# Optimization experiments

Measured on AMD Instinct MI355X. Metric: run time of the kernel, lower is better.

The kernel has to match this reference:

```python
import jax, jax.numpy as jnp
import numpy as np

D_MODEL = 1024
N_HEADS = 16
HEAD_DIM = D_MODEL // N_HEADS
D_FF = 4096
LN_EPS = 1e-5


def _layernorm(x, g, b):
    mu = jnp.mean(x, axis=-1, keepdims=True)
    var = jnp.var(x, axis=-1, keepdims=True)
    return (x - mu) * jax.lax.rsqrt(var + LN_EPS) * g + b


def setup_inputs() -> dict:
    key = jax.random.key(0)
    ks = jax.random.split(key, 10)
    s = 0.02
    return {
        "hidden_states": jax.random.normal(ks[0], (2, 2048, D_MODEL), dtype=jnp.float32),
        "qkv_w": jax.random.normal(ks[1], (3 * D_MODEL, D_MODEL), dtype=jnp.float32) * s,
        "qkv_b": jnp.zeros((3 * D_MODEL,), dtype=jnp.float32),
        "out_w": jax.random.normal(ks[2], (D_MODEL, D_MODEL), dtype=jnp.float32) * s,
        "out_b": jnp.zeros((D_MODEL,), dtype=jnp.float32),
        "fc1_w": jax.random.normal(ks[3], (D_FF, D_MODEL), dtype=jnp.float32) * s,
        "fc1_b": jnp.zeros((D_FF,), dtype=jnp.float32),
        "fc2_w": jax.random.normal(ks[4], (D_MODEL, D_FF), dtype=jnp.float32) * s,
        "fc2_b": jnp.zeros((D_MODEL,), dtype=jnp.float32),
        "ln1_g": jnp.ones((D_MODEL,), dtype=jnp.float32),
        "ln1_b": jnp.zeros((D_MODEL,), dtype=jnp.float32),
        "ln2_g": jnp.ones((D_MODEL,), dtype=jnp.float32),
        "ln2_b": jnp.zeros((D_MODEL,), dtype=jnp.float32),
    }


def reference(hidden_states, qkv_w, qkv_b, out_w, out_b, fc1_w, fc1_b, fc2_w, fc2_b, ln1_g, ln1_b, ln2_g, ln2_b):
    B, S, D = hidden_states.shape
    scale = 1.0 / np.sqrt(HEAD_DIM).astype(np.float32)

    normed = _layernorm(hidden_states, ln1_g, ln1_b)
    qkv = normed @ qkv_w.T + qkv_b  # [B,S,3D]
    qkv = qkv.reshape(B, S, 3, N_HEADS, HEAD_DIM).transpose(2, 0, 3, 1, 4)
    q, k, v = qkv[0], qkv[1], qkv[2]  # [B,H,S,hd]

    scores = jnp.einsum("bhqd,bhkd->bhqk", q, k) * scale
    causal = jnp.tril(jnp.ones((S, S), dtype=bool))
    scores = jnp.where(causal, scores, jnp.float32(-jnp.inf))
    probs = jax.nn.softmax(scores, axis=-1)
    attn = jnp.einsum("bhqk,bhkd->bhqd", probs, v)  # [B,H,S,hd]
    attn = attn.transpose(0, 2, 1, 3).reshape(B, S, D)
    attn = attn @ out_w.T + out_b

    hidden = hidden_states + attn
    normed2 = _layernorm(hidden, ln2_g, ln2_b)
    ff = jax.nn.gelu(normed2 @ fc1_w.T + fc1_b, approximate=False)
    ff = ff @ fc2_w.T + fc2_b
    return hidden + ff
```

## Files before the change

### kernel.cpp

```cpp
#include <hip/hip_runtime.h>
#include <math.h>

using bf16   = __bf16;
using bf16x8 = __attribute__((ext_vector_type(8))) __bf16;
using bf16x4 = __attribute__((ext_vector_type(4))) __bf16;
using f32x4  = __attribute__((ext_vector_type(4))) float;
using f32x16 = __attribute__((ext_vector_type(16))) float;

#define MFMA_16x16x32(a, b, c) __builtin_amdgcn_mfma_f32_16x16x32_bf16((a), (b), (c), 0, 0, 0)
#define MFMA32(a, b, c) __builtin_amdgcn_mfma_f32_32x32x16_bf16((a), (b), (c), 0, 0, 0)

__device__ __forceinline__ void gll16(const void* g, void* l) {
  __builtin_amdgcn_global_load_lds((const __attribute__((address_space(1))) void*)g,
                                   (__attribute__((address_space(3))) void*)l,
                                   16, 0, 0);
}

__device__ __forceinline__ int cvtpk(float lo, float hi) {
  int r;
  asm("v_cvt_pk_bf16_f32 %0, %1, %2" : "=v"(r) : "v"(lo), "v"(hi));
  return r;
}

__global__ __launch_bounds__(256) void cast4_kernel(const float* __restrict__ s0, bf16* d0,
                                                    const float* __restrict__ s1, bf16* d1,
                                                    const float* __restrict__ s2, bf16* d2,
                                                    const float* __restrict__ s3, bf16* d3) {
  int i = blockIdx.x * 256 + threadIdx.x;
  const float* s;
  bf16* d;
  if (i < 786432) { s = s0; d = d0; }
  else if (i < 1048576) { s = s1; d = d1; i -= 786432; }
  else if (i < 2097152) { s = s2; d = d2; i -= 1048576; }
  else { s = s3; d = d3; i -= 2097152; }
  float4 v = ((const float4*)s)[i];
  bf16x4 o;
  o[0] = (bf16)v.x; o[1] = (bf16)v.y; o[2] = (bf16)v.z; o[3] = (bf16)v.w;
  ((bf16x4*)d)[i] = o;
}

__global__ __launch_bounds__(256) void ln_kernel(const float* __restrict__ x,
                                                 const float* __restrict__ g,
                                                 const float* __restrict__ b,
                                                 bf16* __restrict__ out) {
  const int row = blockIdx.x, t = threadIdx.x;
  const float4 v = ((const float4*)(x + (size_t)row * 1024))[t];
  float s1 = v.x + v.y + v.z + v.w;
  float s2 = v.x * v.x + v.y * v.y + v.z * v.z + v.w * v.w;
#pragma unroll
  for (int d = 32; d; d >>= 1) {
    s1 += __shfl_xor(s1, d);
    s2 += __shfl_xor(s2, d);
  }
  __shared__ float red[8];
  const int w = t >> 6;
  if ((t & 63) == 0) { red[w] = s1; red[4 + w] = s2; }
  __syncthreads();
  s1 = red[0] + red[1] + red[2] + red[3];
  s2 = red[4] + red[5] + red[6] + red[7];
  const float mu = s1 * (1.f / 1024.f);
  const float rstd = rsqrtf(s2 * (1.f / 1024.f) - mu * mu + 1e-5f);
  const float4 gv = ((const float4*)g)[t];
  const float4 bv = ((const float4*)b)[t];
  bf16x4 o;
  o[0] = (bf16)((v.x - mu) * rstd * gv.x + bv.x);
  o[1] = (bf16)((v.y - mu) * rstd * gv.y + bv.y);
  o[2] = (bf16)((v.z - mu) * rstd * gv.z + bv.z);
  o[3] = (bf16)((v.w - mu) * rstd * gv.w + bv.w);
  ((bf16x4*)(out + (size_t)row * 1024))[t] = o;
}

template <int EPI>
__global__ __launch_bounds__(512, 2) void gemm256(const bf16* __restrict__ A,
                                                  const bf16* __restrict__ W,
                                                  const float* __restrict__ bias,
                                                  bf16* __restrict__ outp, int N, int K,
                                                  int nbx) {
  __shared__ __align__(1024) bf16 lds[65536];
  const int t = threadIdx.x, lane = t & 63, w = t >> 6;
  const int wm = w >> 2, wn = w & 3;
  const int l15 = lane & 15, lg = lane >> 4;

  const int nwg = gridDim.x, cpx = nwg >> 3, bid = blockIdx.x;
  const int swz = (bid & 7) * cpx + (bid >> 3);
  const int bx = swz % nbx, by = swz / nbx;
  const int m0 = by * 256, n0 = bx * 256;

  const bf16* src[8];
  int dst[8];
  {
    const int ss[2] = {t, t + 512};
#pragma unroll
    for (int i = 0; i < 2; i++) {
      const int d = ss[i] * 16;
      const int L = d ^ (((d >> 9) & 1) << 5);
      const int r = L >> 7, coff = (L & 127) >> 1;
#pragma unroll
      for (int hf = 0; hf < 2; hf++) {
        src[hf * 2 + i]     = A + (size_t)(m0 + hf * 128 + r) * K + coff;
        src[4 + hf * 2 + i] = W + (size_t)(n0 + hf * 128 + r) * K + coff;
        dst[hf * 2 + i]     = hf * 8192 + ss[i] * 8;
        dst[4 + hf * 2 + i] = 16384 + hf * 8192 + ss[i] * 8;
      }
    }
  }

#define STAGE256(db_)                                   \
  do {                                                  \
    _Pragma("unroll") for (int u = 0; u < 8; u++) {     \
      gll16(src[u], lds + (db_)*32768 + dst[u]);        \
      src[u] += 64;                                     \
    }                                                   \
  } while (0)

  f32x4 acc[8][4];
#pragma unroll
  for (int mi = 0; mi < 8; mi++)
#pragma unroll
    for (int ni = 0; ni < 4; ni++) acc[mi][ni] = (f32x4){0.f, 0.f, 0.f, 0.f};

  const int ntiles = K >> 6;
  STAGE256(0);
  asm volatile("s_waitcnt vmcnt(0)" ::: "memory");
  __builtin_amdgcn_s_barrier();

  for (int kt = 0; kt < ntiles; ++kt) {
    const int db = kt & 1;
    const bf16* Ab = lds + db * 32768 + wm * 8192;
    const bf16* Bb = lds + db * 32768 + 16384 + (wn >> 1) * 8192;
    bf16x8 bfr[4][2];
#pragma unroll
    for (int p = 0; p < 4; ++p) {
      bf16x8 af[2][2];
#pragma unroll
      for (int mi2 = 0; mi2 < 2; ++mi2)
#pragma unroll
        for (int ks = 0; ks < 2; ++ks) {
          const int row = (2 * p + mi2) * 16 + l15;
          const int Pb = (row * 128 + ks * 64 + lg * 16) ^ (((row >> 2) & 1) << 5);
          af[mi2][ks] = *(const bf16x8*)((const char*)Ab + Pb);
        }
      if (p == 0) {
#pragma unroll
        for (int ni = 0; ni < 4; ++ni)
#pragma unroll
          for (int ks = 0; ks < 2; ++ks) {
            const int row = (wn & 1) * 64 + ni * 16 + l15;
            const int Pb = (row * 128 + ks * 64 + lg * 16) ^ (((row >> 2) & 1) << 5);
            bfr[ni][ks] = *(const bf16x8*)((const char*)Bb + Pb);
          }
        if (kt + 1 < ntiles) STAGE256(db ^ 1);
      }
      __builtin_amdgcn_s_barrier();
      asm volatile("s_waitcnt lgkmcnt(0)" ::: "memory");
      __builtin_amdgcn_sched_barrier(0);
      __builtin_amdgcn_s_setprio(1);
#pragma unroll
      for (int ks = 0; ks < 2; ++ks)
#pragma unroll
        for (int ni = 0; ni < 4; ++ni) {
          acc[2 * p][ni] = MFMA_16x16x32(af[0][ks], bfr[ni][ks], acc[2 * p][ni]);
          acc[2 * p + 1][ni] = MFMA_16x16x32(af[1][ks], bfr[ni][ks], acc[2 * p + 1][ni]);
        }
      __builtin_amdgcn_s_setprio(0);
      if (p == 3) asm volatile("s_waitcnt vmcnt(0)" ::: "memory");
      __builtin_amdgcn_s_barrier();
    }
  }
#undef STAGE256

#pragma unroll
  for (int mi = 0; mi < 8; ++mi) {
    const int row0 = m0 + wm * 128 + mi * 16 + lg * 4;
#pragma unroll
    for (int ni = 0; ni < 4; ++ni) {
      const int col = n0 + wn * 64 + ni * 16 + l15;
      const float bc = bias[col];
#pragma unroll
      for (int r = 0; r < 4; ++r) {
        float v = acc[mi][ni][r] + bc;
        if (EPI == 1) v = 0.5f * v * (1.f + erff(v * 0.70710678118f));
        outp[(size_t)(row0 + r) * N + col] = (bf16)v;
      }
    }
  }
}

__global__ __launch_bounds__(512, 2) void gemm128(const bf16* __restrict__ A,
                                                  const bf16* __restrict__ W,
                                                  const float* __restrict__ bias,
                                                  const float* __restrict__ resid,
                                                  float* __restrict__ outp, int N, int K,
                                                  int nbx) {
  __shared__ __align__(1024) bf16 lds[65536];
  const int t = threadIdx.x, lane = t & 63, w = t >> 6;
  const int wm = w >> 2, wn = w & 3;
  const int l15 = lane & 15, lg = lane >> 4;

  const int nwg = gridDim.x, cpx = nwg >> 3, bid = blockIdx.x;
  const int swz = (bid & 7) * cpx + (bid >> 3);
  const int bx = swz % nbx, by = swz / nbx;
  const int m0 = by * 128, n0 = bx * 128;

  const bf16* src[8];
  int dst[8];
#pragma unroll
  for (int i = 0; i < 4; i++) {
    const int off = i * 8192 + t * 16;
    const int row = off >> 8, slot = (off >> 4) & 15;
    const int col = (slot ^ (row & 7)) * 8;
    src[i]     = A + (size_t)(m0 + row) * K + col;
    src[4 + i] = W + (size_t)(n0 + row) * K + col;
    dst[i]     = off >> 1;
    dst[4 + i] = 16384 + (off >> 1);
  }

#define STAGE128(db_)                                   \
  do {                                                  \
    _Pragma("unroll") for (int u = 0; u < 8; u++) {     \
      gll16(src[u], lds + (db_)*32768 + dst[u]);        \
      src[u] += 128;                                    \
    }                                                   \
  } while (0)

  f32x4 acc[4][2];
#pragma unroll
  for (int mi = 0; mi < 4; mi++)
#pragma unroll
    for (int ni = 0; ni < 2; ni++) acc[mi][ni] = (f32x4){0.f, 0.f, 0.f, 0.f};

  const int ntiles = K >> 7;
  STAGE128(0);
  asm volatile("s_waitcnt vmcnt(0)" ::: "memory");
  __builtin_amdgcn_s_barrier();

  for (int kt = 0; kt < ntiles; ++kt) {
    const int db = kt & 1;
    const char* Ab = (const char*)(lds + db * 32768);
    const char* Bb = (const char*)(lds + db * 32768 + 16384);
#pragma unroll
    for (int p = 0; p < 4; ++p) {
      bf16x8 af[4], bfr[2];
#pragma unroll
      for (int mi = 0; mi < 4; ++mi) {
        const int row = wm * 64 + mi * 16 + l15;
        af[mi] = *(const bf16x8*)(Ab + row * 256 + (((p * 4 + lg) ^ (row & 7)) << 4));
      }
#pragma unroll
      for (int ni = 0; ni < 2; ++ni) {
        const int row = wn * 32 + ni * 16 + l15;
        bfr[ni] = *(const bf16x8*)(Bb + row * 256 + (((p * 4 + lg) ^ (row & 7)) << 4));
      }
      if (p == 0 && kt + 1 < ntiles) STAGE128(db ^ 1);
      __builtin_amdgcn_s_barrier();
      asm volatile("s_waitcnt lgkmcnt(0)" ::: "memory");
      __builtin_amdgcn_sched_barrier(0);
      __builtin_amdgcn_s_setprio(1);
#pragma unroll
      for (int mi = 0; mi < 4; ++mi)
#pragma unroll
        for (int ni = 0; ni < 2; ++ni)
          acc[mi][ni] = MFMA_16x16x32(af[mi], bfr[ni], acc[mi][ni]);
      __builtin_amdgcn_s_setprio(0);
      if (p == 3) asm volatile("s_waitcnt vmcnt(0)" ::: "memory");
      __builtin_amdgcn_s_barrier();
    }
  }
#undef STAGE128

#pragma unroll
  for (int mi = 0; mi < 4; ++mi) {
    const int row0 = m0 + wm * 64 + mi * 16 + lg * 4;
#pragma unroll
    for (int ni = 0; ni < 2; ++ni) {
      const int col = n0 + wn * 32 + ni * 16 + l15;
      const float bc = bias[col];
#pragma unroll
      for (int r = 0; r < 4; ++r) {
        const size_t idx = (size_t)(row0 + r) * N + col;
        outp[idx] = acc[mi][ni][r] + bc + resid[idx];
      }
    }
  }
}

__global__ __launch_bounds__(256) void vtrans_kernel(const bf16* __restrict__ qkv,
                                                     bf16* __restrict__ vt) {
  __shared__ bf16 tile[64 * 80];
  const int bh = blockIdx.y, b = bh >> 4, h = bh & 15;
  const int s0 = blockIdx.x * 64;
  const int t = threadIdx.x;
#pragma unroll
  for (int c = t; c < 512; c += 256) {
    const int s = c >> 3, d0 = (c & 7) * 8;
    const bf16x8 v =
        *(const bf16x8*)(qkv + (size_t)(b * 2048 + s0 + s) * 3072 + 2048 + h * 64 + d0);
#pragma unroll
    for (int i = 0; i < 8; i++) {
      const int d = d0 + i;
      tile[d * 80 + (s ^ (8 * ((d >> 3) & 7)))] = v[i];
    }
  }
  __syncthreads();
#pragma unroll
  for (int c = t; c < 512; c += 256) {
    const int d = c >> 3, sc = (c & 7) * 8;
    const bf16x8 v = *(const bf16x8*)&tile[d * 80 + (sc ^ (8 * ((d >> 3) & 7)))];
    *(bf16x8*)(vt + ((size_t)bh * 64 + d) * 2048 + s0 + sc) = v;
  }
}

__global__ __launch_bounds__(256) void attn_kernel(const bf16* __restrict__ qkv,
                                                   const bf16* __restrict__ vt,
                                                   bf16* __restrict__ attn_out) {
  __shared__ bf16 Ks[2][4096];
  __shared__ bf16 Vs[2][4096];
  const int t = threadIdx.x, lane = t & 63, w = t >> 6;
  const int l31 = lane & 31, lh = lane >> 5;
  const int bx = blockIdx.x, by = blockIdx.y;
  const int b = by >> 4, h = by & 15;
  const int g = (bx + by) & 15;
  const int qb = (by < 16) ? g : 15 - g;
  const int qw = qb * 128 + w * 32;
  const int qq = qw + l31;
  const int nt = 2 * qb + 2;

  const float cs = 0.18033688011112042f;

  bf16x8 qf[4];
  {
    const bf16* qp = qkv + (size_t)(b * 2048 + qq) * 3072 + h * 64 + lh * 8;
#pragma unroll
    for (int c = 0; c < 4; ++c) qf[c] = *(const bf16x8*)(qp + c * 16);
  }

  const int r0 = t >> 3, c16 = t & 7;
  const int swsl = 8 * (c16 ^ (r0 & 7));
  const bf16* kp0 = qkv + (size_t)(b * 2048 + r0) * 3072 + 1024 + h * 64 + swsl;
  const bf16* kp1 = qkv + (size_t)(b * 2048 + r0 + 32) * 3072 + 1024 + h * 64 + swsl;
  const bf16* vp0 = vt + ((size_t)by * 64 + r0) * 2048 + swsl;
  const bf16* vp1 = vp0 + (size_t)32 * 2048;

#define ASTAGE(buf)                          \
  do {                                       \
    gll16(kp0, &Ks[buf][t * 8]);             \
    gll16(kp1, &Ks[buf][2048 + t * 8]);      \
    gll16(vp0, &Vs[buf][t * 8]);             \
    gll16(vp1, &Vs[buf][2048 + t * 8]);      \
    kp0 += (size_t)64 * 3072;                \
    kp1 += (size_t)64 * 3072;                \
    vp0 += 64;                               \
    vp1 += 64;                               \
  } while (0)

  const f32x16 z16 = {0.f, 0.f, 0.f, 0.f, 0.f, 0.f, 0.f, 0.f,
                      0.f, 0.f, 0.f, 0.f, 0.f, 0.f, 0.f, 0.f};
  f32x16 oacc0 = z16, oacc1 = z16;
  float lsum = 0.f;

  ASTAGE(0);
  __syncthreads();
  int cur = 0;
  for (int tt = 0; tt < nt; ++tt) {
    const int kv0 = tt * 64;
    if (tt + 1 < nt) ASTAGE(cur ^ 1);
    if (kv0 <= qw + 31) {
      const bf16* kbp = Ks[cur];
      const bf16* vbp = Vs[cur];
      const bool up = (kv0 + 32) <= (qw + 31);
      f32x16 s0v = z16, s1v = z16;
      __builtin_amdgcn_s_setprio(1);
#pragma unroll
      for (int c = 0; c < 4; ++c) {
        const int slot = ((c * 2 + lh) ^ (l31 & 7)) * 16;
        const bf16x8 a0 = *(const bf16x8*)((const char*)kbp + l31 * 128 + slot);
        s0v = MFMA32(a0, qf[c], s0v);
      }
      if (up) {
#pragma unroll
        for (int c = 0; c < 4; ++c) {
          const int slot = ((c * 2 + lh) ^ (l31 & 7)) * 16;
          const bf16x8 a1 = *(const bf16x8*)((const char*)kbp + (32 + l31) * 128 + slot);
          s1v = MFMA32(a1, qf[c], s1v);
        }
      }
      __builtin_amdgcn_s_setprio(0);
      if (kv0 + 64 > qw) {
#pragma unroll
        for (int j = 0; j < 16; ++j) {
          const int kr = kv0 + (j & 3) + 8 * (j >> 2) + 4 * lh;
          if (kr > qq) s0v[j] = -1e30f;
          if (kr + 32 > qq) s1v[j] = -1e30f;
        }
      }
#pragma unroll
      for (int j = 0; j < 16; ++j) {
        s0v[j] = exp2f(s0v[j] * cs);
        lsum += s0v[j];
      }
      if (up) {
#pragma unroll
        for (int j = 0; j < 16; ++j) {
          s1v[j] = exp2f(s1v[j] * cs);
          lsum += s1v[j];
        }
      }
      int w0[8], x0[8];
#pragma unroll
      for (int j = 0; j < 8; ++j) w0[j] = cvtpk(s0v[2 * j], s0v[2 * j + 1]);
#pragma unroll
      for (int j = 0; j < 8; ++j) x0[j] = __shfl_xor(w0[j], 32);
#define PVHALF(WW, XX, KB)                                                        \
  do {                                                                            \
    _Pragma("unroll") for (int cc = 0; cc < 2; ++cc) {                            \
      union { int i[4]; bf16x8 v; } pf;                                           \
      pf.i[0] = lh ? XX[4 * cc + 2] : WW[4 * cc + 0];                             \
      pf.i[1] = lh ? XX[4 * cc + 3] : WW[4 * cc + 1];                             \
      pf.i[2] = lh ? WW[4 * cc + 2] : XX[4 * cc + 0];                             \
      pf.i[3] = lh ? WW[4 * cc + 3] : XX[4 * cc + 1];                             \
      const int slot = (((KB)*4 + cc * 2 + lh) ^ (l31 & 7)) * 16;                 \
      const bf16x8 v0 = *(const bf16x8*)((const char*)vbp + l31 * 128 + slot);    \
      const bf16x8 v1 = *(const bf16x8*)((const char*)vbp + (32 + l31) * 128 + slot); \
      oacc0 = MFMA32(v0, pf.v, oacc0);                                            \
      oacc1 = MFMA32(v1, pf.v, oacc1);                                            \
    }                                                                             \
  } while (0)
      __builtin_amdgcn_s_setprio(1);
      PVHALF(w0, x0, 0);
      __builtin_amdgcn_s_setprio(0);
      if (up) {
        int w1[8], x1[8];
#pragma unroll
        for (int j = 0; j < 8; ++j) w1[j] = cvtpk(s1v[2 * j], s1v[2 * j + 1]);
#pragma unroll
        for (int j = 0; j < 8; ++j) x1[j] = __shfl_xor(w1[j], 32);
        __builtin_amdgcn_s_setprio(1);
        PVHALF(w1, x1, 1);
        __builtin_amdgcn_s_setprio(0);
      }
#undef PVHALF
    }
    __syncthreads();
    cur ^= 1;
  }
#undef ASTAGE

  lsum += __shfl_xor(lsum, 32);
  const float rinv = 1.f / lsum;
  bf16* op = attn_out + (size_t)(b * 2048 + qq) * 1024 + h * 64;
#pragma unroll
  for (int gR = 0; gR < 4; ++gR) {
    bf16x4 o0, o1;
#pragma unroll
    for (int r = 0; r < 4; ++r) {
      o0[r] = (bf16)(oacc0[4 * gR + r] * rinv);
      o1[r] = (bf16)(oacc1[4 * gR + r] * rinv);
    }
    *(bf16x4*)(op + 8 * gR + 4 * lh) = o0;
    *(bf16x4*)(op + 32 + 8 * gR + 4 * lh) = o1;
  }
}

extern "C" void kernel_launch(void* const* d_in, const int* in_sizes, int n_in,
                              void* d_out, int out_size, void* d_ws, size_t ws_size,
                              hipStream_t stream) {
  (void)in_sizes; (void)n_in; (void)out_size; (void)ws_size;
  const float* hidden = (const float*)d_in[0];
  const float* qkv_w  = (const float*)d_in[1];
  const float* qkv_b  = (const float*)d_in[2];
  const float* out_w  = (const float*)d_in[3];
  const float* out_b  = (const float*)d_in[4];
  const float* fc1_w  = (const float*)d_in[5];
  const float* fc1_b  = (const float*)d_in[6];
  const float* fc2_w  = (const float*)d_in[7];
  const float* fc2_b  = (const float*)d_in[8];
  const float* ln1_g  = (const float*)d_in[9];
  const float* ln1_b  = (const float*)d_in[10];
  const float* ln2_g  = (const float*)d_in[11];
  const float* ln2_b  = (const float*)d_in[12];
  float* outp = (float*)d_out;

  char* ws = (char*)d_ws;
  bf16*  ln1o = (bf16*)(ws);
  bf16*  qkvb = (bf16*)(ws + ((size_t)8 << 20));
  bf16*  vtb  = (bf16*)(ws + ((size_t)32 << 20));
  bf16*  atto = (bf16*)(ws + ((size_t)40 << 20));
  float* res1 = (float*)(ws + ((size_t)48 << 20));
  bf16*  ln2o = (bf16*)(ws + ((size_t)64 << 20));
  bf16*  ff1  = (bf16*)(ws + ((size_t)72 << 20));
  bf16*  wqkv = (bf16*)(ws + ((size_t)104 << 20));
  bf16*  wout = (bf16*)(ws + ((size_t)110 << 20));
  bf16*  wfc1 = (bf16*)(ws + ((size_t)112 << 20));
  bf16*  wfc2 = (bf16*)(ws + ((size_t)120 << 20));

  cast4_kernel<<<12288, 256, 0, stream>>>(qkv_w, wqkv, out_w, wout, fc1_w, wfc1, fc2_w, wfc2);

  ln_kernel<<<4096, 256, 0, stream>>>(hidden, ln1_g, ln1_b, ln1o);
  gemm256<0><<<192, 512, 0, stream>>>(ln1o, wqkv, qkv_b, qkvb, 3072, 1024, 12);
  vtrans_kernel<<<dim3(32, 32), 256, 0, stream>>>(qkvb, vtb);
  attn_kernel<<<dim3(16, 32), 256, 0, stream>>>(qkvb, vtb, atto);
  gemm128<<<256, 512, 0, stream>>>(atto, wout, out_b, hidden, res1, 1024, 1024, 8);
  ln_kernel<<<4096, 256, 0, stream>>>(res1, ln2_g, ln2_b, ln2o);
  gemm256<1><<<256, 512, 0, stream>>>(ln2o, wfc1, fc1_b, ff1, 4096, 1024, 16);
  gemm128<<<256, 512, 0, stream>>>(ff1, wfc2, fc2_b, res1, outp, 1024, 4096, 8);
}
```

Baseline: 255.6 us.

## Fuse V transpose into QKV GEMM, triple-buffer attention, shrink gemm128 K-tile

The QKV GEMM epilogue now writes the V columns straight into the transposed per-head layout, so the separate vtrans kernel and its extra read and write of V are gone. The attention kernel moves from a double-buffered to a triple-buffered K/V pipeline, with vmcnt-based waits in place of a full __syncthreads each iteration. It also builds the P operand with permlane32_swap instead of eight shuffles per half. gemm128 halves its K tile to 64 to cut LDS use and raises the occupancy hint to 4 blocks per CU, in exchange for more loop iterations and barriers.

```diff
diff --git a/kernel.cpp b/kernel.cpp
--- a/kernel.cpp
+++ b/kernel.cpp
@@ -6,6 +6,7 @@
 using bf16x4 = __attribute__((ext_vector_type(4))) __bf16;
 using f32x4  = __attribute__((ext_vector_type(4))) float;
 using f32x16 = __attribute__((ext_vector_type(16))) float;
+using uint2v = __attribute__((ext_vector_type(2))) unsigned int;
 
 #define MFMA_16x16x32(a, b, c) __builtin_amdgcn_mfma_f32_16x16x32_bf16((a), (b), (c), 0, 0, 0)
 #define MFMA32(a, b, c) __builtin_amdgcn_mfma_f32_32x32x16_bf16((a), (b), (c), 0, 0, 0)
@@ -74,7 +75,8 @@
 __global__ __launch_bounds__(512, 2) void gemm256(const bf16* __restrict__ A,
                                                   const bf16* __restrict__ W,
                                                   const float* __restrict__ bias,
-                                                  bf16* __restrict__ outp, int N, int K,
+                                                  bf16* __restrict__ outp,
+                                                  bf16* __restrict__ vout, int N, int K,
                                                   int nbx) {
   __shared__ __align__(1024) bf16 lds[65536];
   const int t = threadIdx.x, lane = t & 63, w = t >> 6;
@@ -176,23 +178,31 @@
     for (int ni = 0; ni < 4; ++ni) {
       const int col = n0 + wn * 64 + ni * 16 + l15;
       const float bc = bias[col];
-#pragma unroll
-      for (int r = 0; r < 4; ++r) {
-        float v = acc[mi][ni][r] + bc;
-        if (EPI == 1) v = 0.5f * v * (1.f + erff(v * 0.70710678118f));
-        outp[(size_t)(row0 + r) * N + col] = (bf16)v;
-      }
-    }
-  }
-}
-
-__global__ __launch_bounds__(512, 2) void gemm128(const bf16* __restrict__ A,
+      if (EPI == 0 && col >= 2048) {
+        bf16x4 ov;
+#pragma unroll
+        for (int r = 0; r < 4; ++r) ov[r] = (bf16)(acc[mi][ni][r] + bc);
+        const int bb = row0 >> 11, s = row0 & 2047, dc = col - 2048;
+        *(bf16x4*)(vout + ((size_t)(bb * 16 + (dc >> 6)) * 64 + (dc & 63)) * 2048 + s) = ov;
+      } else {
+#pragma unroll
+        for (int r = 0; r < 4; ++r) {
+          float v = acc[mi][ni][r] + bc;
+          if (EPI == 1) v = 0.5f * v * (1.f + erff(v * 0.70710678118f));
+          outp[(size_t)(row0 + r) * N + col] = (bf16)v;
+        }
+      }
+    }
+  }
+}
+
+__global__ __launch_bounds__(512, 4) void gemm128(const bf16* __restrict__ A,
                                                   const bf16* __restrict__ W,
                                                   const float* __restrict__ bias,
                                                   const float* __restrict__ resid,
                                                   float* __restrict__ outp, int N, int K,
                                                   int nbx) {
-  __shared__ __align__(1024) bf16 lds[65536];
+  __shared__ __align__(1024) bf16 lds[32768];
   const int t = threadIdx.x, lane = t & 63, w = t >> 6;
   const int wm = w >> 2, wn = w & 3;
   const int l15 = lane & 15, lg = lane >> 4;
@@ -202,24 +212,24 @@
   const int bx = swz % nbx, by = swz / nbx;
   const int m0 = by * 128, n0 = bx * 128;
 
-  const bf16* src[8];
-  int dst[8];
-#pragma unroll
-  for (int i = 0; i < 4; i++) {
-    const int off = i * 8192 + t * 16;
-    const int row = off >> 8, slot = (off >> 4) & 15;
+  const bf16* src[4];
+  int dst[4];
+#pragma unroll
+  for (int u = 0; u < 2; ++u) {
+    const int off = u * 8192 + t * 16;
+    const int row = off >> 7, slot = (off >> 4) & 7;
     const int col = (slot ^ (row & 7)) * 8;
-    src[i]     = A + (size_t)(m0 + row) * K + col;
-    src[4 + i] = W + (size_t)(n0 + row) * K + col;
-    dst[i]     = off >> 1;
-    dst[4 + i] = 16384 + (off >> 1);
+    src[u]     = A + (size_t)(m0 + row) * K + col;
+    src[2 + u] = W + (size_t)(n0 + row) * K + col;
+    dst[u]     = off >> 1;
+    dst[2 + u] = 8192 + (off >> 1);
   }
 
 #define STAGE128(db_)                                   \
   do {                                                  \
-    _Pragma("unroll") for (int u = 0; u < 8; u++) {     \
-      gll16(src[u], lds + (db_)*32768 + dst[u]);        \
-      src[u] += 128;                                    \
+    _Pragma("unroll") for (int u = 0; u < 4; u++) {     \
+      gll16(src[u], lds + (db_)*16384 + dst[u]);        \
+      src[u] += 64;                                     \
     }                                                   \
   } while (0)
 
@@ -229,27 +239,27 @@
 #pragma unroll
     for (int ni = 0; ni < 2; ni++) acc[mi][ni] = (f32x4){0.f, 0.f, 0.f, 0.f};
 
-  const int ntiles = K >> 7;
+  const int ntiles = K >> 6;
   STAGE128(0);
   asm volatile("s_waitcnt vmcnt(0)" ::: "memory");
   __builtin_amdgcn_s_barrier();
 
   for (int kt = 0; kt < ntiles; ++kt) {
     const int db = kt & 1;
-    const char* Ab = (const char*)(lds + db * 32768);
-    const char* Bb = (const char*)(lds + db * 32768 + 16384);
-#pragma unroll
-    for (int p = 0; p < 4; ++p) {
+    const char* Ab = (const char*)lds + db * 32768;
+    const char* Bb = Ab + 16384;
+#pragma unroll
+    for (int p = 0; p < 2; ++p) {
       bf16x8 af[4], bfr[2];
 #pragma unroll
       for (int mi = 0; mi < 4; ++mi) {
         const int row = wm * 64 + mi * 16 + l15;
-        af[mi] = *(const bf16x8*)(Ab + row * 256 + (((p * 4 + lg) ^ (row & 7)) << 4));
+        af[mi] = *(const bf16x8*)(Ab + row * 128 + (((p * 4 + lg) ^ (row & 7)) << 4));
       }
 #pragma unroll
       for (int ni = 0; ni < 2; ++ni) {
         const int row = wn * 32 + ni * 16 + l15;
-        bfr[ni] = *(const bf16x8*)(Bb + row * 256 + (((p * 4 + lg) ^ (row & 7)) << 4));
+        bfr[ni] = *(const bf16x8*)(Bb + row * 128 + (((p * 4 + lg) ^ (row & 7)) << 4));
       }
       if (p == 0 && kt + 1 < ntiles) STAGE128(db ^ 1);
       __builtin_amdgcn_s_barrier();
@@ -262,7 +272,7 @@
         for (int ni = 0; ni < 2; ++ni)
           acc[mi][ni] = MFMA_16x16x32(af[mi], bfr[ni], acc[mi][ni]);
       __builtin_amdgcn_s_setprio(0);
-      if (p == 3) asm volatile("s_waitcnt vmcnt(0)" ::: "memory");
+      if (p == 1) asm volatile("s_waitcnt vmcnt(0)" ::: "memory");
       __builtin_amdgcn_s_barrier();
     }
   }
@@ -284,37 +294,11 @@
   }
 }
 
-__global__ __launch_bounds__(256) void vtrans_kernel(const bf16* __restrict__ qkv,
-                                                     bf16* __restrict__ vt) {
-  __shared__ bf16 tile[64 * 80];
-  const int bh = blockIdx.y, b = bh >> 4, h = bh & 15;
-  const int s0 = blockIdx.x * 64;
-  const int t = threadIdx.x;
-#pragma unroll
-  for (int c = t; c < 512; c += 256) {
-    const int s = c >> 3, d0 = (c & 7) * 8;
-    const bf16x8 v =
-        *(const bf16x8*)(qkv + (size_t)(b * 2048 + s0 + s) * 3072 + 2048 + h * 64 + d0);
-#pragma unroll
-    for (int i = 0; i < 8; i++) {
-      const int d = d0 + i;
-      tile[d * 80 + (s ^ (8 * ((d >> 3) & 7)))] = v[i];
-    }
-  }
-  __syncthreads();
-#pragma unroll
-  for (int c = t; c < 512; c += 256) {
-    const int d = c >> 3, sc = (c & 7) * 8;
-    const bf16x8 v = *(const bf16x8*)&tile[d * 80 + (sc ^ (8 * ((d >> 3) & 7)))];
-    *(bf16x8*)(vt + ((size_t)bh * 64 + d) * 2048 + s0 + sc) = v;
-  }
-}
-
 __global__ __launch_bounds__(256) void attn_kernel(const bf16* __restrict__ qkv,
                                                    const bf16* __restrict__ vt,
                                                    bf16* __restrict__ attn_out) {
-  __shared__ bf16 Ks[2][4096];
-  __shared__ bf16 Vs[2][4096];
+  __shared__ bf16 Ks[3][4096];
+  __shared__ bf16 Vs[3][4096];
   const int t = threadIdx.x, lane = t & 63, w = t >> 6;
   const int l31 = lane & 31, lh = lane >> 5;
   const int bx = blockIdx.x, by = blockIdx.y;
@@ -359,14 +343,17 @@
   float lsum = 0.f;
 
   ASTAGE(0);
-  __syncthreads();
-  int cur = 0;
+  ASTAGE(1);
+  int b0 = 0, b1 = 1, b2 = 2;
   for (int tt = 0; tt < nt; ++tt) {
     const int kv0 = tt * 64;
-    if (tt + 1 < nt) ASTAGE(cur ^ 1);
+    if (tt < nt - 1) asm volatile("s_waitcnt vmcnt(4)" ::: "memory");
+    else             asm volatile("s_waitcnt vmcnt(0)" ::: "memory");
+    __builtin_amdgcn_s_barrier();
+    if (tt + 2 < nt) ASTAGE(b2);
     if (kv0 <= qw + 31) {
-      const bf16* kbp = Ks[cur];
-      const bf16* vbp = Vs[cur];
+      const bf16* kbp = Ks[b0];
+      const bf16* vbp = Vs[b0];
       const bool up = (kv0 + 32) <= (qw + 31);
       f32x16 s0v = z16, s1v = z16;
       __builtin_amdgcn_s_setprio(1);
@@ -405,43 +392,43 @@
           lsum += s1v[j];
         }
       }
-      int w0[8], x0[8];
-#pragma unroll
-      for (int j = 0; j < 8; ++j) w0[j] = cvtpk(s0v[2 * j], s0v[2 * j + 1]);
-#pragma unroll
-      for (int j = 0; j < 8; ++j) x0[j] = __shfl_xor(w0[j], 32);
-#define PVHALF(WW, XX, KB)                                                        \
-  do {                                                                            \
-    _Pragma("unroll") for (int cc = 0; cc < 2; ++cc) {                            \
-      union { int i[4]; bf16x8 v; } pf;                                           \
-      pf.i[0] = lh ? XX[4 * cc + 2] : WW[4 * cc + 0];                             \
-      pf.i[1] = lh ? XX[4 * cc + 3] : WW[4 * cc + 1];                             \
-      pf.i[2] = lh ? WW[4 * cc + 2] : XX[4 * cc + 0];                             \
-      pf.i[3] = lh ? WW[4 * cc + 3] : XX[4 * cc + 1];                             \
-      const int slot = (((KB)*4 + cc * 2 + lh) ^ (l31 & 7)) * 16;                 \
-      const bf16x8 v0 = *(const bf16x8*)((const char*)vbp + l31 * 128 + slot);    \
-      const bf16x8 v1 = *(const bf16x8*)((const char*)vbp + (32 + l31) * 128 + slot); \
-      oacc0 = MFMA32(v0, pf.v, oacc0);                                            \
-      oacc1 = MFMA32(v1, pf.v, oacc1);                                            \
-    }                                                                             \
+      unsigned int w0[8];
+#pragma unroll
+      for (int j = 0; j < 8; ++j) w0[j] = (unsigned int)cvtpk(s0v[2 * j], s0v[2 * j + 1]);
+#define PVHALF2(WW, KB)                                                              \
+  do {                                                                               \
+    const uint2v e0 = __builtin_amdgcn_permlane32_swap(WW[0], WW[2], false, false);  \
+    const uint2v e1 = __builtin_amdgcn_permlane32_swap(WW[1], WW[3], false, false);  \
+    const uint2v e2 = __builtin_amdgcn_permlane32_swap(WW[4], WW[6], false, false);  \
+    const uint2v e3 = __builtin_amdgcn_permlane32_swap(WW[5], WW[7], false, false);  \
+    union { unsigned int i[4]; bf16x8 v; } pA, pB;                                   \
+    pA.i[0] = e0[0]; pA.i[1] = e1[0]; pA.i[2] = e0[1]; pA.i[3] = e1[1];              \
+    pB.i[0] = e2[0]; pB.i[1] = e3[0]; pB.i[2] = e2[1]; pB.i[3] = e3[1];              \
+    const int sA = (((KB)*4 + lh) ^ (l31 & 7)) * 16;                                 \
+    const int sB = (((KB)*4 + 2 + lh) ^ (l31 & 7)) * 16;                             \
+    const bf16x8 vA0 = *(const bf16x8*)((const char*)vbp + l31 * 128 + sA);          \
+    const bf16x8 vA1 = *(const bf16x8*)((const char*)vbp + (32 + l31) * 128 + sA);   \
+    const bf16x8 vB0 = *(const bf16x8*)((const char*)vbp + l31 * 128 + sB);          \
+    const bf16x8 vB1 = *(const bf16x8*)((const char*)vbp + (32 + l31) * 128 + sB);   \
+    oacc0 = MFMA32(vA0, pA.v, oacc0);                                                \
+    oacc1 = MFMA32(vA1, pA.v, oacc1);                                                \
+    oacc0 = MFMA32(vB0, pB.v, oacc0);                                                \
+    oacc1 = MFMA32(vB1, pB.v, oacc1);                                                \
   } while (0)
       __builtin_amdgcn_s_setprio(1);
-      PVHALF(w0, x0, 0);
+      PVHALF2(w0, 0);
       __builtin_amdgcn_s_setprio(0);
       if (up) {
-        int w1[8], x1[8];
-#pragma unroll
-        for (int j = 0; j < 8; ++j) w1[j] = cvtpk(s1v[2 * j], s1v[2 * j + 1]);
-#pragma unroll
-        for (int j = 0; j < 8; ++j) x1[j] = __shfl_xor(w1[j], 32);
+        unsigned int w1[8];
+#pragma unroll
+        for (int j = 0; j < 8; ++j) w1[j] = (unsigned int)cvtpk(s1v[2 * j], s1v[2 * j + 1]);
         __builtin_amdgcn_s_setprio(1);
-        PVHALF(w1, x1, 1);
+        PVHALF2(w1, 1);
         __builtin_amdgcn_s_setprio(0);
       }
-#undef PVHALF
-    }
-    __syncthreads();
-    cur ^= 1;
+#undef PVHALF2
+    }
+    const int tmp = b0; b0 = b1; b1 = b2; b2 = tmp;
   }
 #undef ASTAGE
 
@@ -496,11 +483,10 @@
   cast4_kernel<<<12288, 256, 0, stream>>>(qkv_w, wqkv, out_w, wout, fc1_w, wfc1, fc2_w, wfc2);
 
   ln_kernel<<<4096, 256, 0, stream>>>(hidden, ln1_g, ln1_b, ln1o);
-  gemm256<0><<<192, 512, 0, stream>>>(ln1o, wqkv, qkv_b, qkvb, 3072, 1024, 12);
-  vtrans_kernel<<<dim3(32, 32), 256, 0, stream>>>(qkvb, vtb);
+  gemm256<0><<<192, 512, 0, stream>>>(ln1o, wqkv, qkv_b, qkvb, vtb, 3072, 1024, 12);
   attn_kernel<<<dim3(16, 32), 256, 0, stream>>>(qkvb, vtb, atto);
   gemm128<<<256, 512, 0, stream>>>(atto, wout, out_b, hidden, res1, 1024, 1024, 8);
   ln_kernel<<<4096, 256, 0, stream>>>(res1, ln2_g, ln2_b, ln2o);
-  gemm256<1><<<256, 512, 0, stream>>>(ln2o, wfc1, fc1_b, ff1, 4096, 1024, 16);
+  gemm256<1><<<256, 512, 0, stream>>>(ln2o, wfc1, fc1_b, ff1, nullptr, 4096, 1024, 16);
   gemm128<<<256, 512, 0, stream>>>(ff1, wfc2, fc2_b, res1, outp, 1024, 4096, 8);
 }
```

Measured after the change: 242.8 us. -5.0%, faster.
